# Optimization experiments

Measured on AMD Instinct MI355X. Metric: run time of the kernel, lower is better.

Reference implementation:

```python
import jax, jax.numpy as jnp
import numpy as np

C = 256
K = 8
D = C // K  # qk projection dim = 32


def setup_inputs() -> dict:
    key = jax.random.key(0)
    ks = jax.random.split(key, 9)
    s = 1.0 / np.sqrt(C)
    x = jax.random.normal(ks[0], (4, C, 64, 64), dtype=jnp.float32)
    Wq = jax.random.normal(ks[1], (D, C), dtype=jnp.float32) * s
    bq = jnp.zeros((D,), dtype=jnp.float32)
    Wk = jax.random.normal(ks[2], (D, C), dtype=jnp.float32) * s
    bk = jnp.zeros((D,), dtype=jnp.float32)
    Wv = jax.random.normal(ks[3], (C, C), dtype=jnp.float32) * s
    bv = jnp.zeros((C,), dtype=jnp.float32)
    Wp = jax.random.normal(ks[4], (C, C), dtype=jnp.float32) * s
    bp = jnp.zeros((C,), dtype=jnp.float32)
    gamma = jnp.float32(0.5)  # nonzero so output depends on attention path
    return {"x": x, "Wq": Wq, "bq": bq, "Wk": Wk, "bk": bk,
            "Wv": Wv, "bv": bv, "Wp": Wp, "bp": bp, "gamma": gamma}


def reference(x, Wq, bq, Wk, bk, Wv, bv, Wp, bp, gamma):
    B, Cc, H, W = x.shape
    N = H * W
    xf = x.reshape(B, Cc, N)  # (B, C, N); 1x1 conv == per-pixel linear
    q = jnp.einsum('dc,bcn->bnd', Wq, xf) + bq  # (B, N, D)
    k = jnp.einsum('dc,bcn->bdn', Wk, xf) + bk[None, :, None]  # (B, D, N)
    v = jnp.einsum('dc,bcn->bdn', Wv, xf) + bv[None, :, None]  # (B, C, N)
    scale = 1.0 / jnp.sqrt(jnp.float32(q.shape[-1]))
    attn = jax.nn.softmax(jnp.einsum('bnd,bdm->bnm', q, k) * scale, axis=-1)  # (B, Nq, Nk)
    out = jnp.einsum('bcm,bnm->bcn', v, attn)  # (B, C, Nq)
    out = jnp.einsum('oc,bcn->bon', Wp, out) + bp[None, :, None]
    out = out.reshape(B, Cc, H, W)
    return x + gamma * out
```

## Files before the change

### kernel.cpp

```cpp
#include <hip/hip_runtime.h>
#include <math.h>

#define BB 4
#define CC 256
#define DD 32
#define NN 4096

typedef __attribute__((ext_vector_type(8))) short short8;
typedef __attribute__((ext_vector_type(4))) float floatx4;
typedef __attribute__((ext_vector_type(16))) float floatx16;
typedef __attribute__((ext_vector_type(4))) int intx4;
typedef __attribute__((ext_vector_type(2))) int intx2;

#define SCALEF (0.17677669529663687f * 1.4426950408889634f)

__device__ __forceinline__ ushort f2bf(float f) {
    unsigned int u = __builtin_bit_cast(unsigned int, f);
    u += 0x7FFFu + ((u >> 16) & 1u);
    return (ushort)(u >> 16);
}
__device__ __forceinline__ int pk_trunc(float a, float b) {
    return (int)__builtin_amdgcn_perm(__builtin_bit_cast(unsigned, b),
                                      __builtin_bit_cast(unsigned, a),
                                      0x07060302u);
}
__device__ __forceinline__ float fast_exp2(float x) {
#if __has_builtin(__builtin_amdgcn_exp2f)
    return __builtin_amdgcn_exp2f(x);
#else
    return exp2f(x);
#endif
}
__device__ __forceinline__ void plswap(int& a, int& b) {
#if __has_builtin(__builtin_amdgcn_permlane32_swap)
    intx2 r = __builtin_amdgcn_permlane32_swap(a, b, false, false);
    a = r[0]; b = r[1];
#else
    const int lane = threadIdx.x & 63;
    const bool hi = lane >= 32;
    int a2 = __shfl(a, lane ^ 32);
    int b2 = __shfl(b, lane ^ 32);
    int na = hi ? b2 : a;
    int nb = hi ? b : a2;
    a = na; b = nb;
#endif
}

#define QTP 264
__global__ __launch_bounds__(640) void qkv_fused(
    const float* __restrict__ x,
    const float* __restrict__ Wq, const float* __restrict__ bq,
    const float* __restrict__ Wk, const float* __restrict__ bk,
    const float* __restrict__ Wv, const float* __restrict__ bv,
    const float* __restrict__ Wp, ushort* __restrict__ Wpb,
    ushort* __restrict__ qb, ushort* __restrict__ kb, ushort* __restrict__ vb)
{
    __shared__ ushort tile[64 * QTP];

    const int t = threadIdx.x;
    const int wave = t >> 6;
    const int lane = t & 63;
    const int l15 = lane & 15, qd = lane >> 4;
    const int b = blockIdx.y;
    const int n0 = blockIdx.x * 64;
    const int mt = wave;

    const int bid = blockIdx.y * gridDim.x + blockIdx.x;
    if (bid < 64 && t < 256) {
        const int e = (bid * 256 + t) * 4;
        const int row = e >> 8, col = e & 255;
        const floatx4 w = *(const floatx4*)(Wp + (size_t)row * CC + col);
        int2 d;
        d.x = pk_trunc(w[0], w[1]);
        d.y = pk_trunc(w[2], w[3]);
        *(int2*)(Wpb + (size_t)row * CC + col) = d;
    }

    if (t < 256) {
        const int cl = (t >> 4) * 4;
        const int nl = (t & 15) * 4;
        #pragma unroll
        for (int p = 0; p < 4; ++p) {
            const int cp = p * 64;
            const float* src = x + ((size_t)b * CC + cp + cl) * NN + n0 + nl;
            floatx4 v[4];
            #pragma unroll
            for (int i = 0; i < 4; ++i) v[i] = *(const floatx4*)(src + (size_t)i * NN);
            #pragma unroll
            for (int j = 0; j < 4; ++j) {
                *(int*)&tile[(nl + j) * QTP + cp + cl]     = pk_trunc(v[0][j], v[1][j]);
                *(int*)&tile[(nl + j) * QTP + cp + cl + 2] = pk_trunc(v[2][j], v[3][j]);
            }
        }
    }
    __syncthreads();

    const float* wr[2];
    if (mt == 0) {
        wr[0] = Wq + (size_t)l15 * CC;
        wr[1] = Wq + (size_t)(16 + l15) * CC;
    } else if (mt == 1) {
        wr[0] = Wk + (size_t)l15 * CC;
        wr[1] = Wk + (size_t)(16 + l15) * CC;
    } else {
        wr[0] = Wv + (size_t)((mt - 2) * 32 + l15) * CC;
        wr[1] = Wv + (size_t)((mt - 2) * 32 + 16 + l15) * CC;
    }

    floatx4 z = {0.f, 0.f, 0.f, 0.f};
    floatx4 acc[2][4];
    #pragma unroll
    for (int fm = 0; fm < 2; ++fm)
        #pragma unroll
        for (int fn = 0; fn < 4; ++fn) acc[fm][fn] = z;

    #pragma unroll
    for (int k0 = 0; k0 < CC; k0 += 32) {
        short8 af[2], bfr[4];
        #pragma unroll
        for (int f = 0; f < 2; ++f) {
            const float* p = wr[f] + k0 + qd * 8;
            float w[8];
            #pragma unroll
            for (int j = 0; j < 8; ++j) w[j] = p[j];
            if (mt == 0) {
                #pragma unroll
                for (int j = 0; j < 8; ++j) w[j] *= SCALEF;
            }
            intx4 d;
            d[0] = pk_trunc(w[0], w[1]); d[1] = pk_trunc(w[2], w[3]);
            d[2] = pk_trunc(w[4], w[5]); d[3] = pk_trunc(w[6], w[7]);
            af[f] = __builtin_bit_cast(short8, d);
        }
        #pragma unroll
        for (int fn = 0; fn < 4; ++fn)
            bfr[fn] = *(const short8*)&tile[(fn * 16 + l15) * QTP + k0 + qd * 8];
        #pragma unroll
        for (int fm = 0; fm < 2; ++fm)
            #pragma unroll
            for (int fn = 0; fn < 4; ++fn)
                acc[fm][fn] = __builtin_amdgcn_mfma_f32_16x16x32_bf16(af[fm], bfr[fn], acc[fm][fn], 0, 0, 0);
    }

    #pragma unroll
    for (int fm = 0; fm < 2; ++fm) {
        const int o0 = fm * 16 + qd * 4;
        if (mt == 0) {
            const floatx4 bb = *(const floatx4*)(bq + o0);
            #pragma unroll
            for (int fn = 0; fn < 4; ++fn) {
                ushort4 h;
                h.x = f2bf(acc[fm][fn][0] + bb[0] * SCALEF);
                h.y = f2bf(acc[fm][fn][1] + bb[1] * SCALEF);
                h.z = f2bf(acc[fm][fn][2] + bb[2] * SCALEF);
                h.w = f2bf(acc[fm][fn][3] + bb[3] * SCALEF);
                *(ushort4*)(qb + ((size_t)b * NN + n0 + fn * 16 + l15) * DD + o0) = h;
            }
        } else if (mt == 1) {
            const floatx4 bb = *(const floatx4*)(bk + o0);
            #pragma unroll
            for (int fn = 0; fn < 4; ++fn) {
                ushort4 h;
                h.x = f2bf(acc[fm][fn][0] + bb[0]);
                h.y = f2bf(acc[fm][fn][1] + bb[1]);
                h.z = f2bf(acc[fm][fn][2] + bb[2]);
                h.w = f2bf(acc[fm][fn][3] + bb[3]);
                *(ushort4*)(kb + (size_t)b * NN * DD
                                 + (size_t)(n0 / 16 + fn) * 512
                                 + (fm * 2 + (qd >> 1)) * 128
                                 + l15 * 8 + (qd & 1) * 4) = h;
            }
        } else {
            const int oc0 = (mt - 2) * 32 + o0;
            const floatx4 bb = *(const floatx4*)(bv + oc0);
            #pragma unroll
            for (int r = 0; r < 4; ++r)
                #pragma unroll
                for (int fn = 0; fn < 4; ++fn)
                    vb[(size_t)b * CC * NN
                       + (size_t)(n0 / 16 + fn) * (CC * 16)
                       + (oc0 + r) * 16 + l15] = f2bf(acc[fm][fn][r] + bb[r]);
        }
    }
}

__global__ __launch_bounds__(256, 2) void attn_mfma(
    const ushort* __restrict__ qb, const ushort* __restrict__ kb,
    const ushort* __restrict__ vb, ushort* __restrict__ aoT)
{
    __shared__ float red[2][8192];
    __shared__ float lred[2][64];

    const int t = threadIdx.x;
    const int kh = t >> 6;
    const int lane = t & 63;
    const int l31 = lane & 31;
    const bool hi = lane >= 32;
    const int hib = hi ? 8 : 0;
    const int slot = blockIdx.x;
    const int b = slot >> 1;
    const int qt = (slot & 1) * 32 + blockIdx.y;
    const int q0 = qt * 64;
    const int c0 = blockIdx.z * 128;

    short8 qf[2][2];
    #pragma unroll
    for (int qg = 0; qg < 2; ++qg)
        #pragma unroll
        for (int dh = 0; dh < 2; ++dh)
            qf[qg][dh] = *(const short8*)(qb + ((size_t)b * NN + q0 + qg * 32 + l31) * DD + dh * 16 + hib);

    const ushort* krow = kb + (size_t)b * NN * DD + (size_t)kh * 64 * 512
                            + (l31 >> 4) * 512 + (l31 & 15) * 8 + hib * 16;
    const ushort* vrow = vb + (size_t)b * CC * NN + (size_t)kh * 64 * (CC * 16)
                            + (c0 + l31) * 16 + hib;

    floatx16 z16 = {0.f,0.f,0.f,0.f,0.f,0.f,0.f,0.f,0.f,0.f,0.f,0.f,0.f,0.f,0.f,0.f};
    floatx16 acc[2][4];
    #pragma unroll
    for (int qg = 0; qg < 2; ++qg)
        #pragma unroll
        for (int cg = 0; cg < 4; ++cg) acc[qg][cg] = z16;
    float lsum[2] = {0.f, 0.f};

    for (int kt = 0; kt < 32; ++kt) {
        short8 kf0 = *(const short8*)(krow);
        short8 kf1 = *(const short8*)(krow + 256);
        krow += 1024;
        short8 vf[4][2];
        #pragma unroll
        for (int cg = 0; cg < 4; ++cg)
            #pragma unroll
            for (int k2 = 0; k2 < 2; ++k2)
                vf[cg][k2] = *(const short8*)(vrow + cg * 512 + k2 * (CC * 16));
        vrow += 2 * (CC * 16);

        short8 ptB[2][2];
        #pragma unroll
        for (int qg = 0; qg < 2; ++qg) {
            floatx16 s = __builtin_amdgcn_mfma_f32_32x32x16_bf16(kf0, qf[qg][0], z16, 0, 0, 0);
            s = __builtin_amdgcn_mfma_f32_32x32x16_bf16(kf1, qf[qg][1], s, 0, 0, 0);

            float e[16];
            #pragma unroll
            for (int r = 0; r < 16; ++r) e[r] = fast_exp2(s[r]);

            lsum[qg] += (((e[0]+e[1])+(e[2]+e[3]))+((e[4]+e[5])+(e[6]+e[7])))
                      + (((e[8]+e[9])+(e[10]+e[11]))+((e[12]+e[13])+(e[14]+e[15])));

            int a0 = pk_trunc(e[0], e[1]),  b0 = pk_trunc(e[2], e[3]);
            int c0w = pk_trunc(e[4], e[5]), d0 = pk_trunc(e[6], e[7]);
            plswap(a0, c0w);
            plswap(b0, d0);
            intx4 f0 = {a0, b0, c0w, d0};
            ptB[qg][0] = __builtin_bit_cast(short8, f0);

            int a1 = pk_trunc(e[8], e[9]),   b1 = pk_trunc(e[10], e[11]);
            int c1 = pk_trunc(e[12], e[13]), d1 = pk_trunc(e[14], e[15]);
            plswap(a1, c1);
            plswap(b1, d1);
            intx4 f1 = {a1, b1, c1, d1};
            ptB[qg][1] = __builtin_bit_cast(short8, f1);
        }

        __builtin_amdgcn_s_setprio(1);
        #pragma unroll
        for (int cg = 0; cg < 4; ++cg)
            #pragma unroll
            for (int qg = 0; qg < 2; ++qg) {
                acc[qg][cg] = __builtin_amdgcn_mfma_f32_32x32x16_bf16(vf[cg][0], ptB[qg][0], acc[qg][cg], 0, 0, 0);
                acc[qg][cg] = __builtin_amdgcn_mfma_f32_32x32x16_bf16(vf[cg][1], ptB[qg][1], acc[qg][cg], 0, 0, 0);
            }
        __builtin_amdgcn_s_setprio(0);
    }

    #pragma unroll
    for (int qg = 0; qg < 2; ++qg)
        lsum[qg] += __shfl(lsum[qg], lane ^ 32);

    if (kh & 1) {
        const int s = kh >> 1;
        #pragma unroll
        for (int qg = 0; qg < 2; ++qg)
            #pragma unroll
            for (int cg = 0; cg < 4; ++cg)
                #pragma unroll
                for (int r = 0; r < 16; ++r)
                    red[s][((qg * 4 + cg) * 16 + r) * 64 + lane] = acc[qg][cg][r];
        if (!hi)
            #pragma unroll
            for (int qg = 0; qg < 2; ++qg) lred[s][qg * 32 + l31] = lsum[qg];
    }
    __syncthreads();
    if (!(kh & 1)) {
        const int s = kh >> 1;
        #pragma unroll
        for (int qg = 0; qg < 2; ++qg) {
            #pragma unroll
            for (int cg = 0; cg < 4; ++cg)
                #pragma unroll
                for (int r = 0; r < 16; ++r)
                    acc[qg][cg][r] += red[s][((qg * 4 + cg) * 16 + r) * 64 + lane];
            lsum[qg] += lred[s][qg * 32 + l31];
        }
    }
    __syncthreads();
    if (kh == 2) {
        #pragma unroll
        for (int qg = 0; qg < 2; ++qg)
            #pragma unroll
            for (int cg = 0; cg < 4; ++cg)
                #pragma unroll
                for (int r = 0; r < 16; ++r)
                    red[0][((qg * 4 + cg) * 16 + r) * 64 + lane] = acc[qg][cg][r];
        if (!hi)
            #pragma unroll
            for (int qg = 0; qg < 2; ++qg) lred[0][qg * 32 + l31] = lsum[qg];
    }
    __syncthreads();
    if (kh == 0) {
        #pragma unroll
        for (int qg = 0; qg < 2; ++qg) {
            #pragma unroll
            for (int cg = 0; cg < 4; ++cg)
                #pragma unroll
                for (int r = 0; r < 16; ++r)
                    acc[qg][cg][r] += red[0][((qg * 4 + cg) * 16 + r) * 64 + lane];
            lsum[qg] += lred[0][qg * 32 + l31];
        }
        #pragma unroll
        for (int qg = 0; qg < 2; ++qg) {
            const float inv = 1.0f / lsum[qg];
            ushort* dst = aoT + ((size_t)b * NN + q0 + qg * 32 + l31) * CC + c0;
            #pragma unroll
            for (int cg = 0; cg < 4; ++cg) {
                #pragma unroll
                for (int rq = 0; rq < 4; ++rq) {
                    ushort4 h;
                    h.x = f2bf(acc[qg][cg][rq * 4 + 0] * inv);
                    h.y = f2bf(acc[qg][cg][rq * 4 + 1] * inv);
                    h.z = f2bf(acc[qg][cg][rq * 4 + 2] * inv);
                    h.w = f2bf(acc[qg][cg][rq * 4 + 3] * inv);
                    *(ushort4*)(dst + cg * 32 + rq * 8 + (hi ? 4 : 0)) = h;
                }
            }
        }
    }
}

__global__ __launch_bounds__(256) void proj_mfma(
    const ushort* __restrict__ aoT, const ushort* __restrict__ Wpb,
    const float* __restrict__ bp, const float* __restrict__ x,
    const float* __restrict__ gamma, float* __restrict__ out)
{
    const int t = threadIdx.x;
    const int wave = t >> 6;
    const int lane = t & 63;
    const int l15 = lane & 15;
    const int qd = lane >> 4;
    const int b = blockIdx.z;
    const int m0 = blockIdx.y * 32;
    const int n0 = blockIdx.x * 128 + wave * 32;

    floatx4 z = {0.f, 0.f, 0.f, 0.f};
    floatx4 acc[2][2];
    acc[0][0] = z; acc[0][1] = z; acc[1][0] = z; acc[1][1] = z;

    const ushort* arow = aoT + ((size_t)b * NN + n0 + l15) * CC + qd * 8;
    const ushort* wrow = Wpb + (size_t)(m0 + l15) * CC + qd * 8;

    #pragma unroll
    for (int k0 = 0; k0 < CC; k0 += 32) {
        short8 af[2], bfr[2];
        af[0]  = *(const short8*)(wrow + k0);
        af[1]  = *(const short8*)(wrow + 16 * CC + k0);
        bfr[0] = *(const short8*)(arow + k0);
        bfr[1] = *(const short8*)(arow + 16 * CC + k0);
        #pragma unroll
        for (int fm = 0; fm < 2; ++fm)
            #pragma unroll
            for (int fn = 0; fn < 2; ++fn)
                acc[fm][fn] = __builtin_amdgcn_mfma_f32_16x16x32_bf16(af[fm], bfr[fn], acc[fm][fn], 0, 0, 0);
    }

    const float g = gamma[0];
    #pragma unroll
    for (int fm = 0; fm < 2; ++fm) {
        #pragma unroll
        for (int r = 0; r < 4; ++r) {
            int m = m0 + fm * 16 + qd * 4 + r;
            float bpv = bp[m];
            #pragma unroll
            for (int fn = 0; fn < 2; ++fn) {
                size_t addr = ((size_t)b * CC + m) * NN + n0 + fn * 16 + l15;
                out[addr] = fmaf(g, acc[fm][fn][r] + bpv, x[addr]);
            }
        }
    }
}

extern "C" void kernel_launch(void* const* d_in, const int* in_sizes, int n_in,
                              void* d_out, int out_size, void* d_ws, size_t ws_size,
                              hipStream_t stream)
{
    const float* x     = (const float*)d_in[0];
    const float* Wq    = (const float*)d_in[1];
    const float* bq    = (const float*)d_in[2];
    const float* Wk    = (const float*)d_in[3];
    const float* bk    = (const float*)d_in[4];
    const float* Wv    = (const float*)d_in[5];
    const float* bv    = (const float*)d_in[6];
    const float* Wp    = (const float*)d_in[7];
    const float* bp    = (const float*)d_in[8];
    const float* gamma = (const float*)d_in[9];
    float* out = (float*)d_out;

    ushort* qbw = (ushort*)d_ws;
    ushort* kbw = qbw + (size_t)BB * NN * DD;
    ushort* vbw = kbw + (size_t)BB * NN * DD;
    ushort* aoT = vbw + (size_t)BB * CC * NN;
    ushort* Wpb = aoT + (size_t)BB * NN * CC;

    qkv_fused<<<dim3(NN / 64, BB), 640, 0, stream>>>(x, Wq, bq, Wk, bk, Wv, bv, Wp, Wpb, qbw, kbw, vbw);
    attn_mfma<<<dim3(8, 32, 2), 256, 0, stream>>>(qbw, kbw, vbw, aoT);
    proj_mfma<<<dim3(NN / 128, CC / 32, BB), 256, 0, stream>>>(aoT, Wpb, bp, x, gamma, out);
}
```

Before: 162.2 us.

## Store attention output and Wp in channel-blocked layout for coalesced proj loads

Changes the bf16 attention output and packed Wp layouts from row-major [n][c] to blocks of 8 channels ([c/8][n][8]). In the projection GEMM, the 16 lanes of each fragment load then read one contiguous span instead of rows strided by 256 channels. The x-tile load in the first kernel is also split across 512 threads, each handling two channel slabs instead of four. The attention kernel's output stores become more scattered, a possible extra cost.

```diff
diff --git a/kernel.cpp b/kernel.cpp
--- a/kernel.cpp
+++ b/kernel.cpp
@@ -73,15 +73,17 @@
         int2 d;
         d.x = pk_trunc(w[0], w[1]);
         d.y = pk_trunc(w[2], w[3]);
-        *(int2*)(Wpb + (size_t)row * CC + col) = d;
-    }
-
-    if (t < 256) {
-        const int cl = (t >> 4) * 4;
-        const int nl = (t & 15) * 4;
-        #pragma unroll
-        for (int p = 0; p < 4; ++p) {
-            const int cp = p * 64;
+        *(int2*)(Wpb + (size_t)(col >> 3) * (CC * 8) + row * 8 + (col & 7)) = d;
+    }
+
+    if (t < 512) {
+        const int tt = t & 255;
+        const int cl = (tt >> 4) * 4;
+        const int nl = (tt & 15) * 4;
+        const int pb = (t >> 8) * 2;
+        #pragma unroll
+        for (int pp = 0; pp < 2; ++pp) {
+            const int cp = (pb + pp) * 64;
             const float* src = x + ((size_t)b * CC + cp + cl) * NN + n0 + nl;
             floatx4 v[4];
             #pragma unroll
@@ -331,7 +333,8 @@
         #pragma unroll
         for (int qg = 0; qg < 2; ++qg) {
             const float inv = 1.0f / lsum[qg];
-            ushort* dst = aoT + ((size_t)b * NN + q0 + qg * 32 + l31) * CC + c0;
+            const int n = q0 + qg * 32 + l31;
+            ushort* dstb = aoT + (size_t)b * NN * CC;
             #pragma unroll
             for (int cg = 0; cg < 4; ++cg) {
                 #pragma unroll
@@ -341,7 +344,8 @@
                     h.y = f2bf(acc[qg][cg][rq * 4 + 1] * inv);
                     h.z = f2bf(acc[qg][cg][rq * 4 + 2] * inv);
                     h.w = f2bf(acc[qg][cg][rq * 4 + 3] * inv);
-                    *(ushort4*)(dst + cg * 32 + rq * 8 + (hi ? 4 : 0)) = h;
+                    *(ushort4*)(dstb + (size_t)(c0 / 8 + cg * 4 + rq) * (NN * 8)
+                                     + (size_t)n * 8 + (hi ? 4 : 0)) = h;
                 }
             }
         }
@@ -366,16 +370,16 @@
     floatx4 acc[2][2];
     acc[0][0] = z; acc[0][1] = z; acc[1][0] = z; acc[1][1] = z;
 
-    const ushort* arow = aoT + ((size_t)b * NN + n0 + l15) * CC + qd * 8;
-    const ushort* wrow = Wpb + (size_t)(m0 + l15) * CC + qd * 8;
+    const ushort* ab = aoT + (size_t)b * NN * CC;
 
     #pragma unroll
     for (int k0 = 0; k0 < CC; k0 += 32) {
+        const size_t cblk = (size_t)(k0 / 8 + qd);
         short8 af[2], bfr[2];
-        af[0]  = *(const short8*)(wrow + k0);
-        af[1]  = *(const short8*)(wrow + 16 * CC + k0);
-        bfr[0] = *(const short8*)(arow + k0);
-        bfr[1] = *(const short8*)(arow + 16 * CC + k0);
+        af[0]  = *(const short8*)(Wpb + cblk * (CC * 8) + (m0 + l15) * 8);
+        af[1]  = *(const short8*)(Wpb + cblk * (CC * 8) + (m0 + 16 + l15) * 8);
+        bfr[0] = *(const short8*)(ab + cblk * (NN * 8) + (size_t)(n0 + l15) * 8);
+        bfr[1] = *(const short8*)(ab + cblk * (NN * 8) + (size_t)(n0 + 16 + l15) * 8);
         #pragma unroll
         for (int fm = 0; fm < 2; ++fm)
             #pragma unroll
```

Result: faster. 152.9 us (-5.7%).
